# Optimization experiments

Hardware: AMD Instinct MI355X
Metric: run time of the kernel (lower is better)

Reference implementation:

```python
import jax, jax.numpy as jnp
import numpy as np

N = 4096
D = 256
L = 4
B = 8


def _graph_norm(x, cums, gamma, beta_g, num_segments):
    # GraphNormGAT: per-graph mean / unbiased std over ragged segments.
    n = x.shape[0]
    seg = jnp.searchsorted(cums, jnp.arange(n), side='right') - 1  # [N] segment ids
    ones = jnp.ones((n,), x.dtype)
    cnt = jax.ops.segment_sum(ones, seg, num_segments=num_segments)[:, None]  # [B,1]
    mean = jax.ops.segment_sum(x, seg, num_segments=num_segments) / cnt       # [B,D]
    diff = x - mean[seg]
    var = jax.ops.segment_sum(diff * diff, seg, num_segments=num_segments) / jnp.maximum(cnt - 1.0, 1.0)
    std = jnp.sqrt(var)
    return gamma * (diff / (std[seg] + 1e-5)) + beta_g


def _mean_shift(beta, xyz, q, k, v, y_hat, mask, t, bw, use_std_att, self_distance, max_iter):
    # Distance-masked mean-shift attention: Gaussian kernel on coordinates
    # combined with QK attention; iteratively shifts xyz toward weighted mean.
    d = q.shape[-1]
    x_out = v
    for _ in range(max_iter):
        att = (q @ k.T) * (1.0 / (np.sqrt(d) * float(t)))  # [N,N]
        if use_std_att:
            m = att.mean(axis=-1, keepdims=True)
            s = att.std(axis=-1, keepdims=True)
            att = (att - m) / (s + 1e-5)
        sq = jnp.sum(xyz * xyz, axis=-1)
        d2 = jnp.maximum(sq[:, None] + sq[None, :] - 2.0 * (xyz @ xyz.T), 0.0)
        d2 = d2 + float(self_distance) * jnp.eye(xyz.shape[0], dtype=d2.dtype)
        logits = att - d2 / (2.0 * bw * bw) + jnp.log(y_hat.T + 1e-9)
        logits = jnp.where(mask, logits, -1e9)
        w = jax.nn.softmax(logits, axis=-1)  # [N,N]
        xyz = beta * (w @ xyz) + (1.0 - beta) * xyz
        x_out = w @ v
    return xyz, x_out


def setup_inputs() -> dict:
    key = jax.random.key(0)
    ks = jax.random.split(key, 12)
    inp = {}
    inp['xyz'] = jax.random.normal(ks[0], (N, 3), jnp.float32)
    inp['x'] = jax.random.normal(ks[1], (N, D), jnp.float32)
    inp['y_hat'] = jax.random.uniform(ks[2], (N, 1), jnp.float32)
    inp['distance_mask'] = jax.random.randint(ks[3], (N, N), 0, 2).astype(bool)
    inp['t'] = 1
    inp['band_width'] = jnp.ones((1,), jnp.float32)
    inp['beta'] = jax.random.uniform(ks[4], (1,), jnp.float32)
    inp['cums'] = jnp.arange(B + 1, dtype=jnp.int32) * (N // B)
    inp['big_inter_mask'] = jnp.ones((N, N), dtype=bool)
    inp['use_std_att'] = 1
    inp['self_distance'] = 10000
    scale = 1.0 / np.sqrt(D)
    inp['qw'] = jax.random.normal(ks[5], (L, D, D), jnp.float32) * scale
    inp['kw'] = jax.random.normal(ks[6], (L, D, D), jnp.float32) * scale
    inp['vw'] = jax.random.normal(ks[7], (L, D, D), jnp.float32) * scale
    inp['ow'] = jax.random.normal(ks[8], (L, D, D), jnp.float32) * scale
    inp['qb'] = jnp.zeros((L, D), jnp.float32)
    inp['kb'] = jnp.zeros((L, D), jnp.float32)
    inp['vb'] = jnp.zeros((L, D), jnp.float32)
    inp['ob'] = jnp.zeros((L, D), jnp.float32)
    inp['gamma'] = jnp.ones((L, 1, D), jnp.float32)
    inp['beta_g'] = jnp.zeros((L, 1, D), jnp.float32)
    return inp


def reference(xyz, x, y_hat, distance_mask, t, band_width, beta, cums,
              big_inter_mask, use_std_att, self_distance,
              qw, kw, vw, ow, qb, kb, vb, ob, gamma, beta_g):
    mask = distance_mask & big_inter_mask
    bw = band_width[0]
    bt = beta[0]
    for l in range(L):
        res = x
        q = x @ qw[l].T + qb[l]
        k = x @ kw[l].T + kb[l]
        v = x @ vw[l].T + vb[l]
        xyz, h = _mean_shift(bt, xyz, q, k, v, y_hat, mask, t, bw,
                             use_std_att, self_distance, max_iter=1)
        h = h @ ow[l].T + ob[l]
        x = res + h
        x = _graph_norm(x, cums, gamma[l], beta_g[l], num_segments=B)
    return x
```

## Files before the change

kernel.cpp:

```cpp
#include <hip/hip_runtime.h>
#include <hip/hip_bf16.h>
#include <math.h>

#define N_ROWS 4096
#define DIM    256
#define LDQ    288
#define NLAYER 4
#define GN_CHUNKS 16

typedef __attribute__((ext_vector_type(8))) short bf16x8;
typedef __attribute__((ext_vector_type(4))) float f32x4;
typedef unsigned short us;

__device__ __forceinline__ us f2b(float f) {
  unsigned int u = __float_as_uint(f);
  unsigned int r = (u + 0x7fffu + ((u >> 16) & 1u)) >> 16;
  return (us)r;
}
__device__ __forceinline__ float b2f(us b) {
  return __uint_as_float(((unsigned int)b) << 16);
}
__device__ __forceinline__ bf16x8 f8_to_b8(float4 a, float4 b) {
  bf16x8 r;
  r[0] = (short)f2b(a.x);
  r[1] = (short)f2b(a.y);
  r[2] = (short)f2b(a.z);
  r[3] = (short)f2b(a.w);
  r[4] = (short)f2b(b.x);
  r[5] = (short)f2b(b.y);
  r[6] = (short)f2b(b.z);
  r[7] = (short)f2b(b.w);
  return r;
}

__global__ __launch_bounds__(256) void mfma_nt_kernel(
    const us* __restrict__ A, int lda, const us* __restrict__ Bb,
    const float* __restrict__ Bf, const float* __restrict__ bias,
    const float* __restrict__ res, float* __restrict__ C) {
  __shared__ __align__(16) short Al[64 * 32];
  __shared__ __align__(16) short Bl[64 * 32];
  const int tid = threadIdx.x;
  const int wv = tid >> 6, lane = tid & 63;
  const int cl = lane & 15, gq = lane >> 4;
  const int wr = wv >> 1, wc = wv & 1;
  const int m0 = blockIdx.x * 64, n0 = blockIdx.y * 64;
  f32x4 acc[2][2];
#pragma unroll
  for (int mi = 0; mi < 2; ++mi)
#pragma unroll
    for (int ni = 0; ni < 2; ++ni) acc[mi][ni] = (f32x4){0.f, 0.f, 0.f, 0.f};
  for (int k0 = 0; k0 < DIM; k0 += 32) {
    __syncthreads();
    {
      int r = tid >> 2, c = tid & 3;
      *(bf16x8*)&Al[r * 32 + c * 8] =
          *(const bf16x8*)&A[(size_t)(m0 + r) * lda + k0 + c * 8];
      if (Bf) {
        float4 u = *(const float4*)&Bf[(size_t)(n0 + r) * DIM + k0 + c * 8];
        float4 v =
            *(const float4*)&Bf[(size_t)(n0 + r) * DIM + k0 + c * 8 + 4];
        *(bf16x8*)&Bl[r * 32 + c * 8] = f8_to_b8(u, v);
      } else {
        *(bf16x8*)&Bl[r * 32 + c * 8] =
            *(const bf16x8*)&Bb[(size_t)(n0 + r) * DIM + k0 + c * 8];
      }
    }
    __syncthreads();
    bf16x8 af[2], bfr[2];
#pragma unroll
    for (int mi = 0; mi < 2; ++mi)
      af[mi] = *(const bf16x8*)&Al[(wr * 32 + mi * 16 + cl) * 32 + gq * 8];
#pragma unroll
    for (int ni = 0; ni < 2; ++ni)
      bfr[ni] = *(const bf16x8*)&Bl[(wc * 32 + ni * 16 + cl) * 32 + gq * 8];
#pragma unroll
    for (int mi = 0; mi < 2; ++mi)
#pragma unroll
      for (int ni = 0; ni < 2; ++ni)
        acc[mi][ni] = __builtin_amdgcn_mfma_f32_16x16x32_bf16(
            af[mi], bfr[ni], acc[mi][ni], 0, 0, 0);
  }
#pragma unroll
  for (int mi = 0; mi < 2; ++mi)
#pragma unroll
    for (int ni = 0; ni < 2; ++ni)
#pragma unroll
      for (int i = 0; i < 4; ++i) {
        int row = m0 + wr * 32 + mi * 16 + gq * 4 + i;
        int col = n0 + wc * 32 + ni * 16 + cl;
        float v = acc[mi][ni][i];
        if (bias) v += bias[col];
        if (res) v += res[(size_t)row * DIM + col];
        C[(size_t)row * DIM + col] = v;
      }
}

__global__ __launch_bounds__(256) void mfma_qkv_kernel(
    const float* __restrict__ A, const float* __restrict__ W0,
    const float* __restrict__ W1, const float* __restrict__ W2,
    const float* __restrict__ b0, const float* __restrict__ b1,
    const float* __restrict__ b2, us* __restrict__ O0, us* __restrict__ O1,
    us* __restrict__ O2) {
  const float* Bm = (blockIdx.z == 0) ? W0 : (blockIdx.z == 1) ? W1 : W2;
  const float* bias = (blockIdx.z == 0) ? b0 : (blockIdx.z == 1) ? b1 : b2;
  us* Ob = (blockIdx.z == 0) ? O0 : (blockIdx.z == 1) ? O1 : O2;
  const int ldo = (blockIdx.z == 2) ? DIM : LDQ;
  __shared__ __align__(16) short Al[64 * 32];
  __shared__ __align__(16) short Bl[64 * 32];
  const int tid = threadIdx.x;
  const int wv = tid >> 6, lane = tid & 63;
  const int cl = lane & 15, gq = lane >> 4;
  const int wr = wv >> 1, wc = wv & 1;
  const int m0 = blockIdx.x * 64, n0 = blockIdx.y * 64;
  f32x4 acc[2][2];
#pragma unroll
  for (int mi = 0; mi < 2; ++mi)
#pragma unroll
    for (int ni = 0; ni < 2; ++ni) acc[mi][ni] = (f32x4){0.f, 0.f, 0.f, 0.f};
  for (int k0 = 0; k0 < DIM; k0 += 32) {
    __syncthreads();
    {
      int r = tid >> 2, c = tid & 3;
      float4 ua = *(const float4*)&A[(size_t)(m0 + r) * DIM + k0 + c * 8];
      float4 va = *(const float4*)&A[(size_t)(m0 + r) * DIM + k0 + c * 8 + 4];
      *(bf16x8*)&Al[r * 32 + c * 8] = f8_to_b8(ua, va);
      float4 ub = *(const float4*)&Bm[(size_t)(n0 + r) * DIM + k0 + c * 8];
      float4 vb = *(const float4*)&Bm[(size_t)(n0 + r) * DIM + k0 + c * 8 + 4];
      *(bf16x8*)&Bl[r * 32 + c * 8] = f8_to_b8(ub, vb);
    }
    __syncthreads();
    bf16x8 af[2], bfr[2];
#pragma unroll
    for (int mi = 0; mi < 2; ++mi)
      af[mi] = *(const bf16x8*)&Al[(wr * 32 + mi * 16 + cl) * 32 + gq * 8];
#pragma unroll
    for (int ni = 0; ni < 2; ++ni)
      bfr[ni] = *(const bf16x8*)&Bl[(wc * 32 + ni * 16 + cl) * 32 + gq * 8];
#pragma unroll
    for (int mi = 0; mi < 2; ++mi)
#pragma unroll
      for (int ni = 0; ni < 2; ++ni)
        acc[mi][ni] = __builtin_amdgcn_mfma_f32_16x16x32_bf16(
            af[mi], bfr[ni], acc[mi][ni], 0, 0, 0);
  }
#pragma unroll
  for (int mi = 0; mi < 2; ++mi)
#pragma unroll
    for (int ni = 0; ni < 2; ++ni)
#pragma unroll
      for (int i = 0; i < 4; ++i) {
        int row = m0 + wr * 32 + mi * 16 + gq * 4 + i;
        int col = n0 + wc * 32 + ni * 16 + cl;
        Ob[(size_t)row * ldo + col] = f2b(acc[mi][ni][i] + bias[col]);
      }
}

__global__ __launch_bounds__(256) void mpart_mfma_kernel(
    const us* __restrict__ Kt, float* __restrict__ Mp) {
  __shared__ __align__(16) short Al[64 * 32];
  __shared__ __align__(16) short Bl[64 * 32];
  const int tid = threadIdx.x;
  const int wv = tid >> 6, lane = tid & 63;
  const int cl = lane & 15, gq = lane >> 4;
  const int wr = wv >> 1, wc = wv & 1;
  const int a0 = blockIdx.x * 64, b0 = blockIdx.y * 64;
  const int kb = blockIdx.z * 512;
  f32x4 acc[2][2];
#pragma unroll
  for (int mi = 0; mi < 2; ++mi)
#pragma unroll
    for (int ni = 0; ni < 2; ++ni) acc[mi][ni] = (f32x4){0.f, 0.f, 0.f, 0.f};
  for (int k0 = 0; k0 < 512; k0 += 32) {
    __syncthreads();
    {
      int r = tid >> 2, c = tid & 3;
      *(bf16x8*)&Al[r * 32 + c * 8] =
          *(const bf16x8*)&Kt[(size_t)(a0 + r) * N_ROWS + kb + k0 + c * 8];
      *(bf16x8*)&Bl[r * 32 + c * 8] =
          *(const bf16x8*)&Kt[(size_t)(b0 + r) * N_ROWS + kb + k0 + c * 8];
    }
    __syncthreads();
    bf16x8 af[2], bfr[2];
#pragma unroll
    for (int mi = 0; mi < 2; ++mi)
      af[mi] = *(const bf16x8*)&Al[(wr * 32 + mi * 16 + cl) * 32 + gq * 8];
#pragma unroll
    for (int ni = 0; ni < 2; ++ni)
      bfr[ni] = *(const bf16x8*)&Bl[(wc * 32 + ni * 16 + cl) * 32 + gq * 8];
#pragma unroll
    for (int mi = 0; mi < 2; ++mi)
#pragma unroll
      for (int ni = 0; ni < 2; ++ni)
        acc[mi][ni] = __builtin_amdgcn_mfma_f32_16x16x32_bf16(
            af[mi], bfr[ni], acc[mi][ni], 0, 0, 0);
  }
#pragma unroll
  for (int mi = 0; mi < 2; ++mi)
#pragma unroll
    for (int ni = 0; ni < 2; ++ni)
#pragma unroll
      for (int i = 0; i < 4; ++i) {
        int row = a0 + wr * 32 + mi * 16 + gq * 4 + i;
        int col = b0 + wc * 32 + ni * 16 + cl;
        Mp[(size_t)blockIdx.z * 65536 + (size_t)row * DIM + col] =
            acc[mi][ni][i];
      }
}

__global__ void mreduce_kernel(const float* __restrict__ Mp,
                               us* __restrict__ Mb) {
  int e = blockIdx.x * 256 + threadIdx.x;
  float s = 0.f;
#pragma unroll
  for (int z = 0; z < 8; ++z) s += Mp[(size_t)z * 65536 + e];
  Mb[e] = f2b(s);
}

__global__ void ksum_part_kernel(const us* __restrict__ K,
                                 float* __restrict__ kpart) {
  int d = threadIdx.x, b = blockIdx.x;
  float s = 0.f;
  int base = b * 64;
  for (int n = 0; n < 64; ++n) s += b2f(K[(size_t)(base + n) * LDQ + d]);
  kpart[b * DIM + d] = s;
}
__global__ void ksum_red_kernel(const float* __restrict__ kpart,
                                float* __restrict__ ksum) {
  int d = threadIdx.x;
  float s = 0.f;
  for (int b = 0; b < 64; ++b) s += kpart[b * DIM + d];
  ksum[d] = s;
}

__global__ __launch_bounds__(256) void stats_kernel(
    us* __restrict__ Qh, us* __restrict__ Kh, us* __restrict__ Vtb,
    const float* __restrict__ tb, const float* __restrict__ ksum,
    const float* __restrict__ xyzc, const float* __restrict__ logy,
    const int* __restrict__ tptr, const float* __restrict__ bwp,
    const int* __restrict__ usestdp, float* __restrict__ c1a,
    float* __restrict__ cAa, float* __restrict__ colB) {
  const int wave = threadIdx.x >> 6, lane = threadIdx.x & 63;
  const int row = blockIdx.x * 4 + wave;
  ushort4 q4 = *(const ushort4*)&Qh[(size_t)row * LDQ + lane * 4];
  float qx = b2f(q4.x), qy = b2f(q4.y), qz = b2f(q4.z), qw = b2f(q4.w);
  const float4 tv4 = ((const float4*)(tb + (size_t)row * DIM))[lane];
  const float4 kv = ((const float4*)ksum)[lane];
  float p1 = qx * kv.x + qy * kv.y + qz * kv.z + qw * kv.w;
  float p2 = tv4.x * qx + tv4.y * qy + tv4.z * qz + tv4.w * qw;
#pragma unroll
  for (int off = 32; off >= 1; off >>= 1) {
    p1 += __shfl_xor(p1, off);
    p2 += __shfl_xor(p2, off);
  }
  float tt = (float)tptr[0];
  float sc = 1.f / (16.f * tt);
  float mean = p1 * sc * (1.f / (float)N_ROWS);
  float e2 = p2 * sc * sc * (1.f / (float)N_ROWS);
  float var = fmaxf(e2 - mean * mean, 0.f);
  float istd = 1.f / (sqrtf(var) + 1e-5f);
  int usestd = usestdp[0];
  float c1 = usestd ? sc * istd : sc;
  float c2 = usestd ? -mean * istd : 0.f;
  float bw = bwp[0];
  float i2 = 1.f / (2.f * bw * bw);
  float t2 = 2.f * i2;
  float x0 = xyzc[(size_t)row * 3 + 0];
  float x1 = xyzc[(size_t)row * 3 + 1];
  float x2 = xyzc[(size_t)row * 3 + 2];
  float sq = x0 * x0 + x1 * x1 + x2 * x2;
  if (lane == 0) {
    c1a[row] = c1;
    cAa[row] = c2 - sq * i2;
    colB[row] = logy[row] - sq * i2;
  }
  float qs = t2 / c1;
  if (lane < 32) {
    float v = (lane == 0) ? qs * x0
              : (lane == 1) ? qs * x1
              : (lane == 2) ? qs * x2
                            : 0.f;
    Qh[(size_t)row * LDQ + 256 + lane] = (lane < 3) ? f2b(v) : 0;
  } else {
    int j = lane - 32;
    float v = (j == 0) ? x0 : (j == 1) ? x1 : (j == 2) ? x2 : 0.f;
    Kh[(size_t)row * LDQ + 256 + j] = (j < 3) ? f2b(v) : 0;
  }
  if (lane < 16) {
    us v = 0;
    if (lane == 0) v = f2b(x0);
    else if (lane == 1) v = f2b(x1);
    else if (lane == 2) v = f2b(x2);
    else if (lane == 3) v = 0x3F80;
    Vtb[(size_t)(256 + lane) * N_ROWS + row] = v;
  }
}

__global__ void prep_kernel(const float* __restrict__ yhat,
                            float* __restrict__ logy) {
  int i = blockIdx.x * 256 + threadIdx.x;
  logy[i] = logf(yhat[i] + 1e-9f);
}

__global__ void maskpack_kernel(const int* __restrict__ dmask,
                                const int* __restrict__ bmask,
                                unsigned int* __restrict__ mbits) {
  int gid = blockIdx.x * 256 + threadIdx.x;
  bool v = (dmask[gid] != 0) && (bmask[gid] != 0);
  unsigned long long bal = __ballot(v);
  if ((threadIdx.x & 63) == 0) {
    int w = gid >> 5;
    mbits[w] = (unsigned int)(bal & 0xffffffffu);
    mbits[w + 1] = (unsigned int)(bal >> 32);
  }
}

__global__ __launch_bounds__(256) void vt2_kernel(const us* __restrict__ inK,
                                                  const us* __restrict__ inV,
                                                  us* __restrict__ outK,
                                                  us* __restrict__ outV) {
  __shared__ us T[64][68];
  const us* in = (blockIdx.z == 0) ? inK : inV;
  us* out = (blockIdx.z == 0) ? outK : outV;
  const int lda = (blockIdx.z == 0) ? LDQ : DIM;
  const int n0 = blockIdx.x * 64, d0 = blockIdx.y * 64;
  const int tx = threadIdx.x & 63, ty = threadIdx.x >> 6;
#pragma unroll
  for (int p = 0; p < 16; ++p)
    T[ty + p * 4][tx] = in[(size_t)(n0 + ty + p * 4) * lda + d0 + tx];
  __syncthreads();
#pragma unroll
  for (int p = 0; p < 16; ++p)
    out[(size_t)(d0 + ty + p * 4) * N_ROWS + n0 + tx] = T[tx][ty + p * 4];
}

__global__ __launch_bounds__(256, 2) void flash5_kernel(
    const us* __restrict__ Qh, const us* __restrict__ Kh,
    const us* __restrict__ Vtb, const float* __restrict__ colB,
    const float* __restrict__ c1a, const float* __restrict__ cAa,
    const unsigned int* __restrict__ mbits, const float* __restrict__ bwp,
    const int* __restrict__ selfdp, us* __restrict__ plo, us* __restrict__ phi,
    float* __restrict__ ps, float* __restrict__ paxlo,
    float* __restrict__ paxhi, int cps) {
  __shared__ __align__(16) short Khl[1152 * 8];
  __shared__ __align__(16) short Vhl[1088 * 8];
  __shared__ __align__(16) short Pl[8][512];

  const int tid = threadIdx.x;
  const int wv = tid >> 6, lane = tid & 63;
  const int cl = lane & 15, gq = lane >> 4;
  const int R0 = blockIdx.x * 128 + wv * 32;
  const int split = blockIdx.y;
  const int colbase = split * cps;

  const float bw = bwp[0];
  const float i2 = 1.f / (2.f * bw * bw);
  const float sd2 = (float)selfdp[0] * i2;

  bf16x8 qa[2][9];
#pragma unroll
  for (int rt = 0; rt < 2; ++rt) {
    const bf16x8* qp = (const bf16x8*)(Qh + (size_t)(R0 + rt * 16 + cl) * LDQ);
#pragma unroll
    for (int ks = 0; ks < 9; ++ks) qa[rt][ks] = qp[ks * 4 + gq];
  }
  float c1v[2][4], cAv[2][4];
#pragma unroll
  for (int rt = 0; rt < 2; ++rt)
#pragma unroll
    for (int i = 0; i < 4; ++i) {
      int row = R0 + rt * 16 + gq * 4 + i;
      c1v[rt][i] = c1a[row];
      cAv[rt][i] = cAa[row];
    }
  f32x4 o[2][17];
#pragma unroll
  for (int rt = 0; rt < 2; ++rt)
#pragma unroll
    for (int dt = 0; dt < 17; ++dt) o[rt][dt] = (f32x4){0.f, 0.f, 0.f, 0.f};

  for (int tt = 0; tt < cps; tt += 32) {
    const int t0g = colbase + tt;
    __syncthreads();
#pragma unroll
    for (int p = 0; p < 9; ++p) {
      int L = tid + p * 256;
      if (L < 1152) {
        int ks = L >> 7, ct = (L >> 6) & 1, g = (L >> 4) & 3, c = L & 15;
        *(bf16x8*)&Khl[L * 8] =
            *(const bf16x8*)&Kh[(size_t)(t0g + 2 * c + ct) * LDQ + ks * 32 +
                                g * 8];
      } else if (L < 2240) {
        int L2 = L - 1152;
        int dt = L2 >> 6, g = (L2 >> 4) & 3, c = L2 & 15;
        *(bf16x8*)&Vhl[L2 * 8] =
            *(const bf16x8*)&Vtb[(size_t)(dt * 16 + c) * N_ROWS + t0g + g * 8];
      }
    }
    __syncthreads();

    const int gc0 = t0g + 2 * cl;
    const float cb0 = colB[gc0];
    const float cb1 = colB[gc0 + 1];

#pragma unroll
    for (int rt = 0; rt < 2; ++rt) {
      f32x4 s0 = (f32x4){0.f, 0.f, 0.f, 0.f};
      f32x4 s1 = (f32x4){0.f, 0.f, 0.f, 0.f};
#pragma unroll
      for (int ks = 0; ks < 9; ++ks) {
        bf16x8 kf = *(const bf16x8*)&Khl[(ks * 128 + gq * 16 + cl) * 8];
        s0 = __builtin_amdgcn_mfma_f32_16x16x32_bf16(qa[rt][ks], kf, s0, 0, 0,
                                                     0);
      }
#pragma unroll
      for (int ks = 0; ks < 9; ++ks) {
        bf16x8 kf = *(const bf16x8*)&Khl[(ks * 128 + 64 + gq * 16 + cl) * 8];
        s1 = __builtin_amdgcn_mfma_f32_16x16x32_bf16(qa[rt][ks], kf, s1, 0, 0,
                                                     0);
      }
#pragma unroll
      for (int i = 0; i < 4; ++i) {
        int row = R0 + rt * 16 + gq * 4 + i;
        unsigned int mw = mbits[((size_t)row << 7) + (t0g >> 5)];
        unsigned int pm = (mw >> (2 * cl)) & 3u;
        float lg0 = fmaf(s0[i], c1v[rt][i], cAv[rt][i] + cb0);
        float lg1 = fmaf(s1[i], c1v[rt][i], cAv[rt][i] + cb1);
        if (row == gc0) lg0 -= sd2;
        if (row == gc0 + 1) lg1 -= sd2;
        lg0 = (pm & 1u) ? lg0 : -60.f;
        lg1 = (pm & 2u) ? lg1 : -60.f;
        float p0 = __expf(lg0);
        float p1 = __expf(lg1);
        unsigned int pk =
            (unsigned int)f2b(p0) | ((unsigned int)f2b(p1) << 16);
        *(unsigned int*)&Pl[wv * 2 + rt]
                          [((cl >> 2) * 16 + gq * 4 + i) * 8 + (cl & 3) * 2] =
            pk;
      }
    }
    bf16x8 pf0 = *(const bf16x8*)&Pl[wv * 2 + 0][(gq * 16 + cl) * 8];
    bf16x8 pf1 = *(const bf16x8*)&Pl[wv * 2 + 1][(gq * 16 + cl) * 8];
#pragma unroll
    for (int dt = 0; dt < 17; ++dt) {
      bf16x8 vf = *(const bf16x8*)&Vhl[(dt * 64 + gq * 16 + cl) * 8];
      o[0][dt] = __builtin_amdgcn_mfma_f32_16x16x32_bf16(pf0, vf, o[0][dt], 0,
                                                         0, 0);
      o[1][dt] = __builtin_amdgcn_mfma_f32_16x16x32_bf16(pf1, vf, o[1][dt], 0,
                                                         0, 0);
    }
  }

  us* pb = (split < 8) ? plo : phi;
  float* paxb = (split < 8) ? paxlo : paxhi;
  const int sl = split & 7;
#pragma unroll
  for (int rt = 0; rt < 2; ++rt)
#pragma unroll
    for (int i = 0; i < 4; ++i) {
      int row = R0 + rt * 16 + gq * 4 + i;
#pragma unroll
      for (int dt = 0; dt < 16; ++dt)
        pb[((size_t)sl * N_ROWS + row) * DIM + dt * 16 + cl] =
            f2b(o[rt][dt][i]);
      float aug = o[rt][16][i];
      if (cl < 3)
        paxb[((size_t)sl * N_ROWS + row) * 3 + cl] = aug;
      else if (cl == 3)
        ps[(size_t)split * N_ROWS + row] = aug;
    }
}

__global__ __launch_bounds__(256) void merge_kernel(
    const us* __restrict__ plo, const us* __restrict__ phi,
    const float* __restrict__ ps, const float* __restrict__ paxlo,
    const float* __restrict__ paxhi, const float* __restrict__ xyzc,
    const float* __restrict__ betap, us* __restrict__ xattb,
    float* __restrict__ xyz_out, int nsplit) {
  const int wvl = threadIdx.x >> 6, lane = threadIdx.x & 63;
  const int row = blockIdx.x * 4 + wvl;
  float den = 0.f;
  for (int k = 0; k < nsplit; ++k) den += ps[(size_t)k * N_ROWS + row];
  float inv = 1.f / den;
  float a0 = 0.f, a1 = 0.f, a2 = 0.f, a3 = 0.f;
  float axs = 0.f;
  for (int k = 0; k < nsplit; ++k) {
    const us* pb = (k < 8) ? plo : phi;
    const us* p = &pb[((size_t)(k & 7) * N_ROWS + row) * DIM + lane * 4];
    uint2 u = *(const uint2*)p;
    a0 += __uint_as_float((u.x & 0xffffu) << 16);
    a1 += __uint_as_float(u.x & 0xffff0000u);
    a2 += __uint_as_float((u.y & 0xffffu) << 16);
    a3 += __uint_as_float(u.y & 0xffff0000u);
    if (lane < 3) {
      const float* paxb = (k < 8) ? paxlo : paxhi;
      axs += paxb[((size_t)(k & 7) * N_ROWS + row) * 3 + lane];
    }
  }
  ushort4 ov;
  ov.x = f2b(a0 * inv);
  ov.y = f2b(a1 * inv);
  ov.z = f2b(a2 * inv);
  ov.w = f2b(a3 * inv);
  *(ushort4*)&xattb[(size_t)row * DIM + lane * 4] = ov;
  if (lane < 3) {
    float beta = betap[0];
    xyz_out[(size_t)row * 3 + lane] =
        beta * axs * inv + (1.f - beta) * xyzc[(size_t)row * 3 + lane];
  }
}

__global__ __launch_bounds__(256) void gn_part_kernel(
    const float* __restrict__ X, const int* __restrict__ cums,
    float* __restrict__ gpart) {
  const int seg = blockIdx.x, chunk = blockIdx.y, d = threadIdx.x;
  const int r0 = cums[seg], r1 = cums[seg + 1];
  const int cnt = r1 - r0;
  const int per = (cnt + GN_CHUNKS - 1) / GN_CHUNKS;
  const int a = r0 + chunk * per;
  const int b = min(a + per, r1);
  float s = 0.f, ss = 0.f;
  for (int r = a; r < b; ++r) {
    float v = X[(size_t)r * DIM + d];
    s += v;
    ss += v * v;
  }
  gpart[(((size_t)seg * GN_CHUNKS + chunk) * 2 + 0) * DIM + d] = s;
  gpart[(((size_t)seg * GN_CHUNKS + chunk) * 2 + 1) * DIM + d] = ss;
}

__global__ void gn_red_kernel(const float* __restrict__ gpart,
                              const int* __restrict__ cums,
                              float* __restrict__ gm, float* __restrict__ gi) {
  const int seg = blockIdx.x, d = threadIdx.x;
  float s = 0.f, ss = 0.f;
#pragma unroll
  for (int c = 0; c < GN_CHUNKS; ++c) {
    s += gpart[(((size_t)seg * GN_CHUNKS + c) * 2 + 0) * DIM + d];
    ss += gpart[(((size_t)seg * GN_CHUNKS + c) * 2 + 1) * DIM + d];
  }
  float cnt = (float)(cums[seg + 1] - cums[seg]);
  float mean = s / fmaxf(cnt, 1.f);
  float var = (ss - cnt * mean * mean) / fmaxf(cnt - 1.f, 1.f);
  gm[seg * DIM + d] = mean;
  gi[seg * DIM + d] = 1.f / (sqrtf(fmaxf(var, 0.f)) + 1e-5f);
}

__global__ __launch_bounds__(256) void gn_apply_kernel(
    const float* __restrict__ X, const float* __restrict__ gamma,
    const float* __restrict__ betag, const int* __restrict__ cums, int nseg,
    const float* __restrict__ gm, const float* __restrict__ gi,
    float* __restrict__ Xout, float* __restrict__ ofinal) {
  int idx = blockIdx.x * 256 + threadIdx.x;
  int base = idx * 4;
  int row = base >> 8, d0 = base & 255;
  int seg = 0;
  for (int b = 1; b <= nseg; ++b) seg += (row >= cums[b]) ? 1 : 0;
  float4 x = ((const float4*)X)[idx];
  float xs[4] = {x.x, x.y, x.z, x.w};
  const float* gmp = gm + seg * DIM + d0;
  const float* gip = gi + seg * DIM + d0;
  float o[4];
#pragma unroll
  for (int c = 0; c < 4; ++c)
    o[c] = gamma[d0 + c] * (xs[c] - gmp[c]) * gip[c] + betag[d0 + c];
  float4 ov = {o[0], o[1], o[2], o[3]};
  ((float4*)Xout)[idx] = ov;
  if (ofinal) ((float4*)ofinal)[idx] = ov;
}

extern "C" void kernel_launch(void* const* d_in, const int* in_sizes, int n_in,
                              void* d_out, int out_size, void* d_ws,
                              size_t ws_size, hipStream_t stream) {
  const float* xyz0 = (const float*)d_in[0];
  const float* x0 = (const float*)d_in[1];
  const float* yhat = (const float*)d_in[2];
  const int* dmask = (const int*)d_in[3];
  const int* tptr = (const int*)d_in[4];
  const float* bwp = (const float*)d_in[5];
  const float* betap = (const float*)d_in[6];
  const int* cums = (const int*)d_in[7];
  const int* bmask = (const int*)d_in[8];
  const int* usestdp = (const int*)d_in[9];
  const int* selfdp = (const int*)d_in[10];
  const float* qw = (const float*)d_in[11];
  const float* kw = (const float*)d_in[12];
  const float* vw = (const float*)d_in[13];
  const float* ow = (const float*)d_in[14];
  const float* qbv = (const float*)d_in[15];
  const float* kbv = (const float*)d_in[16];
  const float* vbv = (const float*)d_in[17];
  const float* obv = (const float*)d_in[18];
  const float* gamma = (const float*)d_in[19];
  const float* betag = (const float*)d_in[20];
  float* out = (float*)d_out;
  float* ws = (float*)d_ws;

  const size_t ND = (size_t)N_ROWS * DIM;

  us* Vb16 = (us*)ws;
  float* bt = ws;
  us* plo = (us*)ws;
  us* Qh = (us*)(ws + 4 * ND);
  us* Kh = Qh + (size_t)N_ROWS * LDQ;
  us* Vtb = Kh + (size_t)N_ROWS * LDQ;
  unsigned int* mbits = (unsigned int*)(Vtb + (size_t)272 * N_ROWS);
  float* kpart = (float*)(mbits + (size_t)N_ROWS * 128);
  float* ksum = kpart + 64 * DIM;
  float* c1a = ksum + DIM;
  float* cAa = c1a + N_ROWS;
  float* colB = cAa + N_ROWS;
  float* logy = colB + N_ROWS;
  float* xyzA = logy + N_ROWS;
  float* xyzB = xyzA + 3 * N_ROWS;
  float* gm = xyzB + 3 * N_ROWS;
  float* gi = gm + 8 * DIM;
  float* gpart = gi + 8 * DIM;
  float* psbase = gpart + 8 * GN_CHUNKS * 2 * DIM;
  float* paxlo = psbase + 16 * (size_t)N_ROWS;
  float* paxhi = paxlo + 8 * (size_t)N_ROWS * 3;
  us* Mb16 = (us*)(paxhi + 8 * (size_t)N_ROWS * 3);
  float* Pend = (float*)(Mb16 + 65536);
  float* bo = Pend;
  us* Ktb = (us*)(bo + ND);
  float* Mp = (float*)(Ktb + (size_t)256 * N_ROWS);
  us* phi = (us*)Pend;
  us* xattb = Ktb;
  const size_t P0w = (size_t)(Pend - ws);
  const size_t full16 = (P0w + 5 * ND) * 4;
  const int nsplit = (ws_size >= full16) ? 16 : 8;
  const int cps = N_ROWS / nsplit;
  float* bx = Pend + (size_t)(nsplit == 16 ? 4 : 2) * ND;

  const int nseg = in_sizes[7] - 1;

  prep_kernel<<<16, 256, 0, stream>>>(yhat, logy);
  maskpack_kernel<<<65536, 256, 0, stream>>>(dmask, bmask, mbits);

  for (int l = 0; l < NLAYER; ++l) {
    const float* xin = (l == 0) ? x0 : bx;
    const float* xyz_in = (l == 0) ? xyz0 : ((l & 1) ? xyzB : xyzA);
    float* xyz_o = (l & 1) ? xyzA : xyzB;
    const size_t wo = (size_t)l * DIM * DIM;

    mfma_qkv_kernel<<<dim3(64, 4, 3), 256, 0, stream>>>(
        xin, qw + wo, kw + wo, vw + wo, qbv + l * DIM, kbv + l * DIM,
        vbv + l * DIM, Qh, Kh, Vb16);
    ksum_part_kernel<<<64, 256, 0, stream>>>(Kh, kpart);
    vt2_kernel<<<dim3(64, 4, 2), 256, 0, stream>>>(Kh, Vb16, Ktb, Vtb);
    ksum_red_kernel<<<1, 256, 0, stream>>>(kpart, ksum);
    mpart_mfma_kernel<<<dim3(4, 4, 8), 256, 0, stream>>>(Ktb, Mp);
    mreduce_kernel<<<256, 256, 0, stream>>>(Mp, Mb16);
    mfma_nt_kernel<<<dim3(64, 4), 256, 0, stream>>>(Qh, LDQ, Mb16, nullptr,
                                                    nullptr, nullptr, bt);
    stats_kernel<<<1024, 256, 0, stream>>>(Qh, Kh, Vtb, bt, ksum, xyz_in, logy,
                                           tptr, bwp, usestdp, c1a, cAa, colB);
    flash5_kernel<<<dim3(32, nsplit), 256, 0, stream>>>(
        Qh, Kh, Vtb, colB, c1a, cAa, mbits, bwp, selfdp, plo, phi, psbase,
        paxlo, paxhi, cps);
    merge_kernel<<<1024, 256, 0, stream>>>(plo, phi, psbase, paxlo, paxhi,
                                           xyz_in, betap, xattb, xyz_o,
                                           nsplit);
    mfma_nt_kernel<<<dim3(64, 4), 256, 0, stream>>>(
        xattb, DIM, nullptr, ow + wo, obv + l * DIM, xin, bo);
    gn_part_kernel<<<dim3(nseg, GN_CHUNKS), 256, 0, stream>>>(bo, cums, gpart);
    gn_red_kernel<<<nseg, 256, 0, stream>>>(gpart, cums, gm, gi);
    gn_apply_kernel<<<1024, 256, 0, stream>>>(
        bo, gamma + (size_t)l * DIM, betag + (size_t)l * DIM, cums, nseg, gm,
        gi, bx, (l == NLAYER - 1) ? out : nullptr);
  }
}
```

Baseline: 777.0 us.

## Prefetch next K/V tile into registers, stage output via LDS, swap grid axes

The flash attention kernel now loads the next K/V tile from global memory into registers while computing on the current tile, then writes it to shared memory after a barrier. This hides global load latency behind the MFMA work. The partial output is written to shared memory first and stored as coalesced 16-byte vectors instead of scattered 2-byte stores. Grid axes are swapped so that blocks for the same row tile with different column splits launch next to each other. The register staging adds pressure and may lower occupancy at 2 blocks per CU.

Result: slower. 936.8 us (+20.6%).

```diff
diff --git a/kernel.cpp b/kernel.cpp
--- a/kernel.cpp
+++ b/kernel.cpp
@@ -341,15 +341,16 @@
     const int* __restrict__ selfdp, us* __restrict__ plo, us* __restrict__ phi,
     float* __restrict__ ps, float* __restrict__ paxlo,
     float* __restrict__ paxhi, int cps) {
-  __shared__ __align__(16) short Khl[1152 * 8];
-  __shared__ __align__(16) short Vhl[1088 * 8];
-  __shared__ __align__(16) short Pl[8][512];
+  __shared__ __align__(16) short SMEM[22016];
+  short* Khl = SMEM;
+  short* Vhl = SMEM + 9216;
+  short* Pl = SMEM + 17920;
 
   const int tid = threadIdx.x;
   const int wv = tid >> 6, lane = tid & 63;
   const int cl = lane & 15, gq = lane >> 4;
-  const int R0 = blockIdx.x * 128 + wv * 32;
-  const int split = blockIdx.y;
+  const int split = blockIdx.x;
+  const int R0 = blockIdx.y * 128 + wv * 32;
   const int colbase = split * cps;
 
   const float bw = bwp[0];
@@ -378,25 +379,42 @@
 #pragma unroll
     for (int dt = 0; dt < 17; ++dt) o[rt][dt] = (f32x4){0.f, 0.f, 0.f, 0.f};
 
-  for (int tt = 0; tt < cps; tt += 32) {
-    const int t0g = colbase + tt;
-    __syncthreads();
+  bf16x8 stg[9];
+  auto load_tile = [&](int t0g) {
 #pragma unroll
     for (int p = 0; p < 9; ++p) {
       int L = tid + p * 256;
       if (L < 1152) {
         int ks = L >> 7, ct = (L >> 6) & 1, g = (L >> 4) & 3, c = L & 15;
-        *(bf16x8*)&Khl[L * 8] =
-            *(const bf16x8*)&Kh[(size_t)(t0g + 2 * c + ct) * LDQ + ks * 32 +
-                                g * 8];
+        stg[p] = *(const bf16x8*)&Kh[(size_t)(t0g + 2 * c + ct) * LDQ +
+                                     ks * 32 + g * 8];
       } else if (L < 2240) {
         int L2 = L - 1152;
         int dt = L2 >> 6, g = (L2 >> 4) & 3, c = L2 & 15;
-        *(bf16x8*)&Vhl[L2 * 8] =
+        stg[p] =
             *(const bf16x8*)&Vtb[(size_t)(dt * 16 + c) * N_ROWS + t0g + g * 8];
       }
     }
-    __syncthreads();
+  };
+  auto write_tile = [&]() {
+#pragma unroll
+    for (int p = 0; p < 9; ++p) {
+      int L = tid + p * 256;
+      if (L < 1152)
+        *(bf16x8*)&Khl[L * 8] = stg[p];
+      else if (L < 2240)
+        *(bf16x8*)&Vhl[(L - 1152) * 8] = stg[p];
+    }
+  };
+
+  load_tile(colbase);
+  write_tile();
+  __syncthreads();
+
+  for (int tt = 0; tt < cps; tt += 32) {
+    const int t0g = colbase + tt;
+    const bool hasnext = (tt + 32 < cps);
+    if (hasnext) load_tile(t0g + 32);
 
     const int gc0 = t0g + 2 * cl;
     const float cb0 = colB[gc0];
@@ -433,13 +451,13 @@
         float p1 = __expf(lg1);
         unsigned int pk =
             (unsigned int)f2b(p0) | ((unsigned int)f2b(p1) << 16);
-        *(unsigned int*)&Pl[wv * 2 + rt]
-                          [((cl >> 2) * 16 + gq * 4 + i) * 8 + (cl & 3) * 2] =
+        *(unsigned int*)&Pl[(wv * 2 + rt) * 512 +
+                            ((cl >> 2) * 16 + gq * 4 + i) * 8 + (cl & 3) * 2] =
             pk;
       }
     }
-    bf16x8 pf0 = *(const bf16x8*)&Pl[wv * 2 + 0][(gq * 16 + cl) * 8];
-    bf16x8 pf1 = *(const bf16x8*)&Pl[wv * 2 + 1][(gq * 16 + cl) * 8];
+    bf16x8 pf0 = *(const bf16x8*)&Pl[(wv * 2 + 0) * 512 + (gq * 16 + cl) * 8];
+    bf16x8 pf1 = *(const bf16x8*)&Pl[(wv * 2 + 1) * 512 + (gq * 16 + cl) * 8];
 #pragma unroll
     for (int dt = 0; dt < 17; ++dt) {
       bf16x8 vf = *(const bf16x8*)&Vhl[(dt * 64 + gq * 16 + cl) * 8];
@@ -448,26 +466,42 @@
       o[1][dt] = __builtin_amdgcn_mfma_f32_16x16x32_bf16(pf1, vf, o[1][dt], 0,
                                                          0, 0);
     }
+    __syncthreads();
+    if (hasnext) {
+      write_tile();
+      __syncthreads();
+    }
   }
 
   us* pb = (split < 8) ? plo : phi;
   float* paxb = (split < 8) ? paxlo : paxhi;
   const int sl = split & 7;
-#pragma unroll
-  for (int rt = 0; rt < 2; ++rt)
+  short* obuf = SMEM + wv * 4096;
+#pragma unroll
+  for (int rt = 0; rt < 2; ++rt) {
+#pragma unroll
+    for (int dt = 0; dt < 16; ++dt)
+#pragma unroll
+      for (int i = 0; i < 4; ++i)
+        obuf[(gq * 4 + i) * 256 + dt * 16 + cl] = (short)f2b(o[rt][dt][i]);
+#pragma unroll
+    for (int p = 0; p < 8; ++p) {
+      int idx = p * 512 + lane * 8;
+      int rl = idx >> 8;
+      int col = idx & 255;
+      bf16x8 v = *(const bf16x8*)&obuf[idx];
+      *(bf16x8*)&pb[((size_t)sl * N_ROWS + R0 + rt * 16 + rl) * DIM + col] = v;
+    }
 #pragma unroll
     for (int i = 0; i < 4; ++i) {
       int row = R0 + rt * 16 + gq * 4 + i;
-#pragma unroll
-      for (int dt = 0; dt < 16; ++dt)
-        pb[((size_t)sl * N_ROWS + row) * DIM + dt * 16 + cl] =
-            f2b(o[rt][dt][i]);
       float aug = o[rt][16][i];
       if (cl < 3)
         paxb[((size_t)sl * N_ROWS + row) * 3 + cl] = aug;
       else if (cl == 3)
         ps[(size_t)split * N_ROWS + row] = aug;
     }
+  }
 }
 
 __global__ __launch_bounds__(256) void merge_kernel(
@@ -654,7 +688,7 @@
                                                     nullptr, nullptr, bt);
     stats_kernel<<<1024, 256, 0, stream>>>(Qh, Kh, Vtb, bt, ksum, xyz_in, logy,
                                            tptr, bwp, usestdp, c1a, cAa, colB);
-    flash5_kernel<<<dim3(32, nsplit), 256, 0, stream>>>(
+    flash5_kernel<<<dim3(nsplit, 32), 256, 0, stream>>>(
         Qh, Kh, Vtb, colB, c1a, cAa, mbits, bwp, selfdp, plo, phi, psbase,
         paxlo, paxhi, cps);
     merge_kernel<<<1024, 256, 0, stream>>>(plo, phi, psbase, paxlo, paxhi,
```
